# Performance work log

Measured on AMD Instinct MI355X. Metric: run time of the kernel, lower is better.

Reference implementation:

```python
import jax, jax.numpy as jnp
import numpy as np

B, T, H, E = 256, 512, 512, 32

def setup_inputs() -> dict:
    key = jax.random.key(0)
    ks = jax.random.split(key, 7)
    events = jax.random.randint(ks[0], (B, T), 0, E, dtype=jnp.int32)
    # strictly increasing event times (as produced by cumsum of positive gaps upstream)
    gaps = jax.random.uniform(ks[1], (B, T), dtype=jnp.float32) * 0.1 + 1e-3
    times = jnp.cumsum(gaps, axis=1)
    emb = jax.random.normal(ks[2], (E, H), dtype=jnp.float32) * 0.05
    # 5 gate Linears (input, forget, output, cell, decay) stacked: [2H, 5H]
    W_gates = jax.random.normal(ks[3], (2 * H, 5 * H), dtype=jnp.float32) * (1.0 / np.sqrt(2 * H))
    b_gates = jnp.zeros((5 * H,), dtype=jnp.float32)
    W_int = jax.random.normal(ks[4], (H, E), dtype=jnp.float32) * (1.0 / np.sqrt(H))
    b_int = jnp.zeros((E,), dtype=jnp.float32)
    return {"events": events, "times": times, "emb": emb,
            "W_gates": W_gates, "b_gates": b_gates, "W_int": W_int, "b_int": b_int}

def reference(events, times, emb, W_gates, b_gates, W_int, b_int):
    Bs, Ts = events.shape
    Hs = emb.shape[1]
    x_seq = emb[events]                                   # [B,T,H] embedding lookup
    deltas = jnp.concatenate([times[:, :1], jnp.diff(times, axis=1)], axis=1)  # [B,T]
    xs = (jnp.transpose(x_seq, (1, 0, 2)), deltas.T)      # ([T,B,H], [T,B])

    def step(carry, inp):
        h, c = carry
        x, dt = inp
        comb = jnp.concatenate([x, h], axis=1)            # [B,2H]
        g = comb @ W_gates + b_gates                      # [B,5H] fused gate GEMM
        i, f, o, c_tilde, d = jnp.split(g, 5, axis=1)
        i, f, o, c_tilde = jnp.tanh(i), jnp.tanh(f), jnp.tanh(o), jnp.tanh(c_tilde)
        decay = jax.nn.softplus(d)
        c_dec = c * jnp.exp(-decay * dt[:, None])
        c_n = f * c_dec + i * c_tilde
        h_n = o * jnp.tanh(c_n)
        lam = jax.nn.softplus(h_n @ W_int + b_int)        # [B,E]
        return (h_n, c_n), (lam, h_n)

    h0 = jnp.zeros((Bs, Hs), dtype=times.dtype)
    c0 = jnp.zeros((Bs, Hs), dtype=times.dtype)
    _, (lams, hs) = jax.lax.scan(step, (h0, c0), xs)
    intensities = jnp.transpose(lams, (1, 0, 2))          # [B,T,E]
    hidden_states = jnp.transpose(hs, (1, 0, 2))          # [B,T,H]
    return intensities, hidden_states
```

## Files before the change

kernel.cpp:

```cpp
#include <hip/hip_runtime.h>
#include <math.h>


#define Bb   256
#define Tt   512
#define Hh   512
#define Ee   32
#define G5H  2560
#define NTHR 256
#define RT   16
#define CT   32

typedef __attribute__((ext_vector_type(8))) short f16x8;
typedef __attribute__((ext_vector_type(4))) float f32x4;

__device__ __forceinline__ float softplusf(float x) {
    return fmaxf(x, 0.f) + __logf(1.f + __expf(-fabsf(x)));
}
__device__ __forceinline__ float fast_tanh(float x) {
    const float t = fminf(fmaxf(x, -15.f), 15.f);
    const float e = __expf(2.f * t);
    return (e - 1.f) / (e + 1.f);
}
__device__ __forceinline__ unsigned short f2h(float f) {
    _Float16 h = (_Float16)f;
    return *reinterpret_cast<unsigned short*>(&h);
}

__device__ __forceinline__ void load_a4(const unsigned short* p, f16x8 (&a)[4]) {
    asm volatile(
        "global_load_dwordx4 %0, %4, off sc0 sc1\n\t"
        "global_load_dwordx4 %1, %4, off offset:64 sc0 sc1\n\t"
        "global_load_dwordx4 %2, %4, off offset:128 sc0 sc1\n\t"
        "global_load_dwordx4 %3, %4, off offset:192 sc0 sc1\n\t"
        "s_waitcnt vmcnt(0)"
        : "=&v"(a[0]), "=&v"(a[1]), "=&v"(a[2]), "=&v"(a[3])
        : "v"(p) : "memory");
}
__device__ __forceinline__ void st_u32_sc(void* p, unsigned v) {
    asm volatile("global_store_dword %0, %1, off sc0 sc1"
                 :: "v"(p), "v"(v) : "memory");
}
__device__ __forceinline__ unsigned ld_u32_sc(const unsigned* p) {
    unsigned v;
    asm volatile("global_load_dword %0, %1, off sc0 sc1\n\ts_waitcnt vmcnt(0)"
                 : "=v"(v) : "v"(p) : "memory");
    return v;
}

__global__ __launch_bounds__(NTHR, 1)
void nhp_scan(const int* __restrict__ events, const float* __restrict__ times,
              const float* __restrict__ emb, const float* __restrict__ Wg,
              const float* __restrict__ bg, float* __restrict__ out_hid,
              unsigned* __restrict__ flags, unsigned short* __restrict__ hb) {
    __shared__ float red[4][10][16][18];
    __shared__ float gx[Ee][5][34];
    __shared__ float dt_lds[RT][516];
    __shared__ unsigned char ev_lds[RT][520];

    const int tid  = threadIdx.x, bid = blockIdx.x;
    const int rt   = bid & 15;
    const int ct   = bid >> 4;
    const int r0   = rt * RT;
    const int lane = tid & 63;
    const int ks   = tid >> 6;
    const int frow = lane & 15, kgrp = lane >> 4;
    const int erow = tid >> 4;
    const int ecp  = (tid & 15) * 2;

    for (int u = tid; u < RT * Tt; u += NTHR) {
        const int row = u >> 9, pp = u & 511;
        const float t1 = times[(r0 + row) * Tt + pp];
        const float t0 = pp ? times[(r0 + row) * Tt + pp - 1] : 0.f;
        dt_lds[row][pp] = t1 - t0;
        ev_lds[row][pp] = (unsigned char)events[(r0 + row) * Tt + pp];
    }

    for (int u = tid; u < Ee * 5 * CT; u += NTHR) {
        const int e = u / 160, r = u - e * 160;
        const int g = r >> 5, hc = r & 31;
        const int gcol = g * Hh + ct * CT + hc;
        float acc = bg[gcol];
        const float* er = emb + (size_t)e * Hh;
        for (int k = 0; k < Hh; k += 4) {
            acc += er[k]     * Wg[(size_t)k       * G5H + gcol];
            acc += er[k + 1] * Wg[(size_t)(k + 1) * G5H + gcol];
            acc += er[k + 2] * Wg[(size_t)(k + 2) * G5H + gcol];
            acc += er[k + 3] * Wg[(size_t)(k + 3) * G5H + gcol];
        }
        gx[e][g][hc ^ ((e & 7) << 2)] = acc;
    }

    f16x8 Bf[10][4];
    #pragma unroll
    for (int n = 0; n < 10; ++n) {
        const int col = (n >> 1) * Hh + ct * CT + (n & 1) * 16 + frow;
        #pragma unroll
        for (int kk = 0; kk < 4; ++kk) {
            const int k0 = ks * 128 + kk * 32 + kgrp * 8;
            union { f16x8 v; unsigned u[4]; } tmp;
            #pragma unroll
            for (int r = 0; r < 4; ++r) {
                const float w0 = Wg[(size_t)(Hh + k0 + 2 * r)     * G5H + col];
                const float w1 = Wg[(size_t)(Hh + k0 + 2 * r + 1) * G5H + col];
                tmp.u[r] = (unsigned)f2h(w0) | ((unsigned)f2h(w1) << 16);
            }
            Bf[n][kk] = tmp.v;
        }
    }

    float cA = 0.f, cB = 0.f;
    __syncthreads();

    for (int p = 0; p < Tt; ++p) {
        if (p > 0) {
            const unsigned* fp = flags + rt * 16 + ks * 4 + (lane & 3);
            const unsigned want = (unsigned)p;
            int guard = 0;
            for (;;) {
                const unsigned fv = ld_u32_sc(fp);
                if (__all(fv >= want)) break;
                if (++guard > 300000) break;
                __builtin_amdgcn_s_sleep(1);
            }

            const unsigned short* hp = hb + (size_t)((p - 1) & 1) * Bb * Hh
                                     + (size_t)(r0 + frow) * Hh + ks * 128 + kgrp * 8;
            f16x8 a[4];
            load_a4(hp, a);

            f32x4 acc[10];
            #pragma unroll
            for (int n = 0; n < 10; ++n) acc[n] = (f32x4){0.f, 0.f, 0.f, 0.f};
            #pragma unroll
            for (int kk = 0; kk < 4; ++kk) {
                #pragma unroll
                for (int n = 0; n < 10; ++n)
                    acc[n] = __builtin_amdgcn_mfma_f32_16x16x32_f16(
                        a[kk], Bf[n][kk], acc[n], 0, 0, 0);
            }
            #pragma unroll
            for (int n = 0; n < 10; ++n)
                #pragma unroll
                for (int r = 0; r < 4; ++r)
                    red[ks][n][kgrp * 4 + r][frow] = acc[n][r];
        }
        __syncthreads();

        const int   e  = ev_lds[erow][p];
        const float dt = dt_lds[erow][p];
        const int   sc = (e & 7) << 2;
        float hn[2];
        {
            float v0[5], v1[5];
            const int tl0 = ecp >> 4, fc = ecp & 15;
            #pragma unroll
            for (int gt = 0; gt < 5; ++gt) {
                const float2 gv = *(const float2*)&gx[e][gt][ecp ^ sc];
                v0[gt] = gv.x; v1[gt] = gv.y;
                if (p > 0) {
                    const int tl = gt * 2 + tl0;
                    #pragma unroll
                    for (int s = 0; s < 4; ++s) {
                        const float2 pr = *(const float2*)&red[s][tl][erow][fc];
                        v0[gt] += pr.x; v1[gt] += pr.y;
                    }
                }
            }
            #pragma unroll
            for (int q = 0; q < 2; ++q) {
                const float* v = q ? v1 : v0;
                const float ig  = fast_tanh(v[0]);
                const float fg  = fast_tanh(v[1]);
                const float og  = fast_tanh(v[2]);
                const float ctl = fast_tanh(v[3]);
                const float dec = softplusf(v[4]);
                const float cpv = q ? cB : cA;
                const float cn  = fg * (cpv * __expf(-dec * dt)) + ig * ctl;
                if (q) cB = cn; else cA = cn;
                hn[q] = og * fast_tanh(cn);
            }
        }

        float2 ho; ho.x = hn[0]; ho.y = hn[1];
        *(float2*)(out_hid + ((size_t)(r0 + erow) * Tt + p) * Hh + ct * CT + ecp) = ho;
        const unsigned pk = (unsigned)f2h(hn[0]) | ((unsigned)f2h(hn[1]) << 16);
        st_u32_sc(hb + (size_t)(p & 1) * Bb * Hh
                     + (size_t)(r0 + erow) * Hh + ct * CT + ecp, pk);

        asm volatile("s_waitcnt vmcnt(0)" ::: "memory");
        __syncthreads();
        if (tid == 0) st_u32_sc(&flags[rt * 16 + ct], (unsigned)(p + 1));
    }
}

__global__ __launch_bounds__(NTHR)
void nhp_intens(const float* __restrict__ out_hid, const float* __restrict__ Wi,
                const float* __restrict__ bi, float* __restrict__ out_int) {
    const int tid  = threadIdx.x;
    const int w    = tid >> 6;
    const int lane = tid & 63;
    const int col  = lane & 15, kgrp = lane >> 4;

    f16x8 Bfi[2][16];
    #pragma unroll
    for (int n = 0; n < 2; ++n)
        #pragma unroll
        for (int kk = 0; kk < 16; ++kk) {
            const int k0 = kk * 32 + kgrp * 8;
            union { f16x8 v; unsigned u[4]; } tmp;
            #pragma unroll
            for (int r = 0; r < 4; ++r) {
                const float w0 = Wi[(size_t)(k0 + 2 * r)     * Ee + n * 16 + col];
                const float w1 = Wi[(size_t)(k0 + 2 * r + 1) * Ee + n * 16 + col];
                tmp.u[r] = (unsigned)f2h(w0) | ((unsigned)f2h(w1) << 16);
            }
            Bfi[n][kk] = tmp.v;
        }
    const float bv[2] = { bi[col], bi[16 + col] };

    #pragma unroll
    for (int it = 0; it < 2; ++it) {
        const size_t rowbase = (size_t)blockIdx.x * 128 + (w * 2 + it) * 16;
        f32x4 acc0 = (f32x4){0.f,0.f,0.f,0.f}, acc1 = acc0;
        #pragma unroll
        for (int kk = 0; kk < 16; ++kk) {
            const float* hp = out_hid + (rowbase + (lane & 15)) * Hh + kk * 32 + kgrp * 8;
            const float4 hA = *(const float4*)hp;
            const float4 hB = *(const float4*)(hp + 4);
            union { f16x8 v; unsigned u[4]; } t;
            t.u[0] = (unsigned)f2h(hA.x) | ((unsigned)f2h(hA.y) << 16);
            t.u[1] = (unsigned)f2h(hA.z) | ((unsigned)f2h(hA.w) << 16);
            t.u[2] = (unsigned)f2h(hB.x) | ((unsigned)f2h(hB.y) << 16);
            t.u[3] = (unsigned)f2h(hB.z) | ((unsigned)f2h(hB.w) << 16);
            acc0 = __builtin_amdgcn_mfma_f32_16x16x32_f16(t.v, Bfi[0][kk], acc0, 0, 0, 0);
            acc1 = __builtin_amdgcn_mfma_f32_16x16x32_f16(t.v, Bfi[1][kk], acc1, 0, 0, 0);
        }
        #pragma unroll
        for (int i = 0; i < 4; ++i) {
            const size_t row = rowbase + kgrp * 4 + i;
            out_int[row * Ee + col]      = softplusf(acc0[i] + bv[0]);
            out_int[row * Ee + 16 + col] = softplusf(acc1[i] + bv[1]);
        }
    }
}

extern "C" void kernel_launch(void* const* d_in, const int* in_sizes, int n_in,
                              void* d_out, int out_size, void* d_ws, size_t ws_size,
                              hipStream_t stream) {
    const int*   events = (const int*)d_in[0];
    const float* times  = (const float*)d_in[1];
    const float* emb    = (const float*)d_in[2];
    const float* Wg     = (const float*)d_in[3];
    const float* bg     = (const float*)d_in[4];
    const float* Wi     = (const float*)d_in[5];
    const float* bi     = (const float*)d_in[6];
    float* out_int = (float*)d_out;
    float* out_hid = out_int + (size_t)Bb * Tt * Ee;
    unsigned* flags = (unsigned*)d_ws;
    unsigned short* hb = (unsigned short*)((char*)d_ws + 4096);

    hipMemsetAsync(flags, 0, 4096, stream);
    hipLaunchKernelGGL(nhp_scan, dim3(256), dim3(NTHR), 0, stream,
                       events, times, emb, Wg, bg, out_hid, flags, hb);
    hipLaunchKernelGGL(nhp_intens, dim3((Bb * Tt) / 128), dim3(NTHR), 0, stream,
                       out_hid, Wi, bi, out_int);
}
```

Measured before the change: 2.266 ms.

## Repartition scan blocks into 8-row groups with 64-column tiles and per-wave flags

The persistent scan kernel now gives each block 8 batch rows and 64 hidden columns across 32 row groups, instead of 16 rows by 32 columns. Each block issues 20 MFMA tiles instead of 10 and uses half of each 16-row tile, padding rows to 16 in the h buffer (zeroed by memset). The change halves the number of peer blocks each block must wait on per step and finer-grains the flags to one per wave, published before the barrier. This aims to cut the cross-block synchronization latency of the serial recurrence, at the cost of wasted MFMA work on the padded rows and more registers for the B fragments.

```diff
diff --git a/kernel.cpp b/kernel.cpp
--- a/kernel.cpp
+++ b/kernel.cpp
@@ -8,8 +8,9 @@
 #define Ee   32
 #define G5H  2560
 #define NTHR 256
-#define RT   16
-#define CT   32
+#define RG   8
+#define CTW  64
+#define NT   20
 
 typedef __attribute__((ext_vector_type(8))) short f16x8;
 typedef __attribute__((ext_vector_type(4))) float f32x4;
@@ -53,22 +54,22 @@
               const float* __restrict__ emb, const float* __restrict__ Wg,
               const float* __restrict__ bg, float* __restrict__ out_hid,
               unsigned* __restrict__ flags, unsigned short* __restrict__ hb) {
-    __shared__ float red[4][10][16][18];
-    __shared__ float gx[Ee][5][34];
-    __shared__ float dt_lds[RT][516];
-    __shared__ unsigned char ev_lds[RT][520];
+    __shared__ float red[4][NT][8][18];
+    __shared__ float gx[Ee][5][68];
+    __shared__ float dt_lds[RG][516];
+    __shared__ unsigned char ev_lds[RG][520];
 
     const int tid  = threadIdx.x, bid = blockIdx.x;
-    const int rt   = bid & 15;
-    const int ct   = bid >> 4;
-    const int r0   = rt * RT;
+    const int g    = bid & 31;
+    const int ct   = bid >> 5;
+    const int r0   = g * RG;
     const int lane = tid & 63;
     const int ks   = tid >> 6;
     const int frow = lane & 15, kgrp = lane >> 4;
-    const int erow = tid >> 4;
-    const int ecp  = (tid & 15) * 2;
-
-    for (int u = tid; u < RT * Tt; u += NTHR) {
+    const int er   = tid >> 5;
+    const int ecl  = (tid & 31) * 2;
+
+    for (int u = tid; u < RG * Tt; u += NTHR) {
         const int row = u >> 9, pp = u & 511;
         const float t1 = times[(r0 + row) * Tt + pp];
         const float t0 = pp ? times[(r0 + row) * Tt + pp - 1] : 0.f;
@@ -76,25 +77,26 @@
         ev_lds[row][pp] = (unsigned char)events[(r0 + row) * Tt + pp];
     }
 
-    for (int u = tid; u < Ee * 5 * CT; u += NTHR) {
-        const int e = u / 160, r = u - e * 160;
-        const int g = r >> 5, hc = r & 31;
-        const int gcol = g * Hh + ct * CT + hc;
+    for (int u = tid; u < Ee * 5 * CTW; u += NTHR) {
+        const int e = u / 320, r = u - e * 320;
+        const int gq = r >> 6, hc = r & 63;
+        const int gcol = gq * Hh + ct * CTW + hc;
         float acc = bg[gcol];
-        const float* er = emb + (size_t)e * Hh;
+        const float* er_ = emb + (size_t)e * Hh;
         for (int k = 0; k < Hh; k += 4) {
-            acc += er[k]     * Wg[(size_t)k       * G5H + gcol];
-            acc += er[k + 1] * Wg[(size_t)(k + 1) * G5H + gcol];
-            acc += er[k + 2] * Wg[(size_t)(k + 2) * G5H + gcol];
-            acc += er[k + 3] * Wg[(size_t)(k + 3) * G5H + gcol];
-        }
-        gx[e][g][hc ^ ((e & 7) << 2)] = acc;
-    }
-
-    f16x8 Bf[10][4];
+            acc += er_[k]     * Wg[(size_t)k       * G5H + gcol];
+            acc += er_[k + 1] * Wg[(size_t)(k + 1) * G5H + gcol];
+            acc += er_[k + 2] * Wg[(size_t)(k + 2) * G5H + gcol];
+            acc += er_[k + 3] * Wg[(size_t)(k + 3) * G5H + gcol];
+        }
+        gx[e][gq][hc ^ ((e & 15) << 2)] = acc;
+    }
+
+    f16x8 Bf[NT][4];
     #pragma unroll
-    for (int n = 0; n < 10; ++n) {
-        const int col = (n >> 1) * Hh + ct * CT + (n & 1) * 16 + frow;
+    for (int n = 0; n < NT; ++n) {
+        const int gq = n >> 2, sub = n & 3;
+        const int col = gq * Hh + ct * CTW + sub * 16 + frow;
         #pragma unroll
         for (int kk = 0; kk < 4; ++kk) {
             const int k0 = ks * 128 + kk * 32 + kgrp * 8;
@@ -114,7 +116,7 @@
 
     for (int p = 0; p < Tt; ++p) {
         if (p > 0) {
-            const unsigned* fp = flags + rt * 16 + ks * 4 + (lane & 3);
+            const unsigned* fp = flags + g * 32 + ks * 8 + (lane & 7);
             const unsigned want = (unsigned)p;
             int guard = 0;
             for (;;) {
@@ -124,45 +126,44 @@
                 __builtin_amdgcn_s_sleep(1);
             }
 
-            const unsigned short* hp = hb + (size_t)((p - 1) & 1) * Bb * Hh
-                                     + (size_t)(r0 + frow) * Hh + ks * 128 + kgrp * 8;
+            const unsigned short* hp = hb
+                + ((size_t)(((p - 1) & 1) * 32 + g) * 16 + frow) * Hh
+                + ks * 128 + kgrp * 8;
             f16x8 a[4];
             load_a4(hp, a);
 
-            f32x4 acc[10];
-            #pragma unroll
-            for (int n = 0; n < 10; ++n) acc[n] = (f32x4){0.f, 0.f, 0.f, 0.f};
-            #pragma unroll
-            for (int kk = 0; kk < 4; ++kk) {
+            #pragma unroll
+            for (int n = 0; n < NT; ++n) {
+                f32x4 acc = (f32x4){0.f, 0.f, 0.f, 0.f};
                 #pragma unroll
-                for (int n = 0; n < 10; ++n)
-                    acc[n] = __builtin_amdgcn_mfma_f32_16x16x32_f16(
-                        a[kk], Bf[n][kk], acc[n], 0, 0, 0);
-            }
-            #pragma unroll
-            for (int n = 0; n < 10; ++n)
-                #pragma unroll
-                for (int r = 0; r < 4; ++r)
-                    red[ks][n][kgrp * 4 + r][frow] = acc[n][r];
+                for (int kk = 0; kk < 4; ++kk)
+                    acc = __builtin_amdgcn_mfma_f32_16x16x32_f16(
+                        a[kk], Bf[n][kk], acc, 0, 0, 0);
+                if (lane < 32) {
+                    #pragma unroll
+                    for (int r = 0; r < 4; ++r)
+                        red[ks][n][kgrp * 4 + r][lane & 15] = acc[r];
+                }
+            }
         }
         __syncthreads();
 
-        const int   e  = ev_lds[erow][p];
-        const float dt = dt_lds[erow][p];
-        const int   sc = (e & 7) << 2;
+        const int   e  = ev_lds[er][p];
+        const float dt = dt_lds[er][p];
+        const int   sw = (e & 15) << 2;
         float hn[2];
         {
             float v0[5], v1[5];
-            const int tl0 = ecp >> 4, fc = ecp & 15;
+            const int fc = ecl & 15, nq = ecl >> 4;
             #pragma unroll
             for (int gt = 0; gt < 5; ++gt) {
-                const float2 gv = *(const float2*)&gx[e][gt][ecp ^ sc];
+                const float2 gv = *(const float2*)&gx[e][gt][ecl ^ sw];
                 v0[gt] = gv.x; v1[gt] = gv.y;
                 if (p > 0) {
-                    const int tl = gt * 2 + tl0;
+                    const int n = gt * 4 + nq;
                     #pragma unroll
                     for (int s = 0; s < 4; ++s) {
-                        const float2 pr = *(const float2*)&red[s][tl][erow][fc];
+                        const float2 pr = *(const float2*)&red[s][n][er][fc];
                         v0[gt] += pr.x; v1[gt] += pr.y;
                     }
                 }
@@ -183,14 +184,15 @@
         }
 
         float2 ho; ho.x = hn[0]; ho.y = hn[1];
-        *(float2*)(out_hid + ((size_t)(r0 + erow) * Tt + p) * Hh + ct * CT + ecp) = ho;
+        *(float2*)(out_hid + ((size_t)(r0 + er) * Tt + p) * Hh + ct * CTW + ecl) = ho;
         const unsigned pk = (unsigned)f2h(hn[0]) | ((unsigned)f2h(hn[1]) << 16);
-        st_u32_sc(hb + (size_t)(p & 1) * Bb * Hh
-                     + (size_t)(r0 + erow) * Hh + ct * CT + ecp, pk);
+        st_u32_sc((unsigned*)hb + (((size_t)((p & 1) * 32 + g) * 16 + er) * 256
+                                   + ct * 32 + (ecl >> 1)), pk);
 
         asm volatile("s_waitcnt vmcnt(0)" ::: "memory");
+        if ((tid & 63) == 0)
+            st_u32_sc(&flags[g * 32 + ct * 4 + ks], (unsigned)(p + 1));
         __syncthreads();
-        if (tid == 0) st_u32_sc(&flags[rt * 16 + ct], (unsigned)(p + 1));
     }
 }
 
@@ -260,7 +262,7 @@
     unsigned* flags = (unsigned*)d_ws;
     unsigned short* hb = (unsigned short*)((char*)d_ws + 4096);
 
-    hipMemsetAsync(flags, 0, 4096, stream);
+    hipMemsetAsync(d_ws, 0, 4096 + (size_t)2 * 32 * 16 * Hh * 2, stream);
     hipLaunchKernelGGL(nhp_scan, dim3(256), dim3(NTHR), 0, stream,
                        events, times, emb, Wg, bg, out_hid, flags, hb);
     hipLaunchKernelGGL(nhp_intens, dim3((Bb * Tt) / 128), dim3(NTHR), 0, stream,
```

Result: slower. 3.355 ms (+48.1%).
